# Performance work log

Measured on AMD Instinct MI355X. Metric: run time of the kernel, lower is better.

The kernel has to match this reference:

```python
import jax, jax.numpy as jnp
import numpy as np


def setup_inputs() -> dict:
    key = jax.random.key(0)
    k1, k2 = jax.random.split(key)
    N, DIM = 32768, 1024
    M, K, D = 8, 1024, 128  # n_quantizer, n_codeword, sub_dim
    x = jax.random.normal(k1, (N, DIM), dtype=jnp.float32)
    CodeBooks = jax.random.uniform(k2, (M, K, D), dtype=jnp.float32)  # torch.rand init
    return {"x": x, "CodeBooks": CodeBooks, "soft_rate": -1}


def reference(x, CodeBooks, soft_rate):
    # x: [N, dim]; CodeBooks: [M, K, D] with dim = M*D
    N = x.shape[0]
    M, K, D = CodeBooks.shape
    # forward detaches x before quantizing
    sx = jax.lax.stop_gradient(x).reshape(-1, M, D)  # [N, M, D]
    # squared euclidean distances for all sub-quantizers at once:
    # d2[n,m,k] = ||sx[n,m] - CB[m,k]||^2
    dots = jnp.einsum("nmd,mkd->nmk", sx, CodeBooks)          # [N, M, K]
    x2 = jnp.sum(sx * sx, axis=-1)                             # [N, M]
    c2 = jnp.sum(CodeBooks * CodeBooks, axis=-1)               # [M, K]
    d2 = x2[:, :, None] + c2[None, :, :] - 2.0 * dots          # [N, M, K]
    if soft_rate == -1:
        # argmax of -dist == argmin of squared dist (sqrt is monotone)
        idx = jnp.argmin(d2, axis=-1)                          # [N, M]
        Q = CodeBooks[jnp.arange(M)[None, :], idx]             # [N, M, D]
    else:
        dist = -jnp.sqrt(jnp.maximum(d2, 0.0))                 # -cdist, p=2
        w = jax.nn.softmax(dist * soft_rate, axis=-1)          # [N, M, K]
        Q = jnp.einsum("nmk,mkd->nmd", w, CodeBooks)           # [N, M, D]
    return Q.reshape(N, M * D)
```

## Files before the change

### kernel.cpp

```cpp
#include <hip/hip_runtime.h>
#include <stdint.h>

#define NROWS   32768
#define XDIM    1024
#define NCB     8
#define NCODE   1024
#define CDIM    128

#define CHUNK   32
#define NCHUNK  (NCODE / CHUNK)

#define NTH     512
#define ROWS_PB 256
#define RPW     32

typedef _Float16 h8 __attribute__((ext_vector_type(8)));
typedef float    f4 __attribute__((ext_vector_type(4)));

#define LO_SCALE 2048.0f
#define LO_INV   4.8828125e-4f

#define WS_HI   ((size_t)0)
#define WS_LO   ((size_t)NCB * NCODE * CDIM * 2)
#define WS_C2   ((size_t)2 * NCB * NCODE * CDIM * 2)
#define WS_NEED (WS_C2 + (size_t)NCB * NCODE * 4)

__device__ __forceinline__ void gload_lds16(const void* g, void* l) {
    __builtin_amdgcn_global_load_lds(
        (const __attribute__((address_space(1))) void*)g,
        (__attribute__((address_space(3))) void*)l, 16, 0, 0);
}

__global__ __launch_bounds__(256)
void precompute_kernel(const float* __restrict__ cb, uint8_t* __restrict__ ws)
{
    _Float16* hi = (_Float16*)(ws + WS_HI);
    _Float16* lo = (_Float16*)(ws + WS_LO);
    float*    c2 = (float*)(ws + WS_C2);

    const int idx  = blockIdx.x * 256 + threadIdx.x;
    const int g    = idx & 15;
    const int code = idx >> 4;
    const int kr   = code & 31;
    const int gs   = g ^ (kr & 7);

    const float* src = cb + (size_t)code * CDIM + gs * 8;
    float v[8];
    *(f4*)&v[0] = *(const f4*)src;
    *(f4*)&v[4] = *(const f4*)(src + 4);

    _Float16 hh[8], ll[8];
    double s = 0.0;
    #pragma unroll
    for (int i = 0; i < 8; ++i) {
        _Float16 h = (_Float16)v[i];
        float    r = v[i] - (float)h;
        hh[i] = h; ll[i] = (_Float16)(r * LO_SCALE);
        s = fma((double)v[i], (double)v[i], s);
    }
    const size_t off = (size_t)code * CDIM + g * 8;
    *(h8*)(hi + off) = *(h8*)hh;
    *(h8*)(lo + off) = *(h8*)ll;

    #pragma unroll
    for (int mask = 1; mask <= 8; mask <<= 1)
        s += __shfl_xor(s, mask, 16);
    if (g == 0) c2[code] = (float)s;
}

__global__ __launch_bounds__(NTH, 4)
void quant_fast(const float* __restrict__ x, const float* __restrict__ cb,
                const uint8_t* __restrict__ ws, float* __restrict__ out)
{
    __shared__ __align__(16) _Float16 chS[2][CHUNK][CDIM];
    __shared__ __align__(16) _Float16 clS[2][CHUNK][CDIM];
    __shared__ float  c2s[NCODE];
    __shared__ float  x2s[ROWS_PB];
    __shared__ int    idxs[ROWS_PB];

    const _Float16* pre_hi = (const _Float16*)(ws + WS_HI);
    const _Float16* pre_lo = (const _Float16*)(ws + WS_LO);
    const float*    c2w    = (const float*)(ws + WS_C2);

    const int t    = threadIdx.x;
    const int m    = blockIdx.x & 7;
    const int rb   = blockIdx.x >> 3;
    const int row0 = rb * ROWS_PB;

    const int l    = t & 63;
    const int w    = t >> 6;
    const int l15  = l & 15;
    const int lh   = l >> 4;
    const int mskr = (l & 7) * 8;

    const size_t cbase = (size_t)m * NCODE * CDIM;

    auto stage = [&](int c, int buf) {
        const _Float16* gh = pre_hi + cbase + (size_t)(c * CHUNK + w * 4) * CDIM + l * 8;
        const _Float16* gl = pre_lo + cbase + (size_t)(c * CHUNK + w * 4) * CDIM + l * 8;
        gload_lds16(gh, &chS[buf][w * 4][0]);
        gload_lds16(gl, &clS[buf][w * 4][0]);
    };

    stage(0, 0);

    if (t < 256) *(f4*)&c2s[t * 4] = *(const f4*)&c2w[m * NCODE + t * 4];

    h8 xh[2][4], xl[2][4];
    #pragma unroll
    for (int rs = 0; rs < 2; ++rs) {
        const float* xp = x + (size_t)(row0 + w * RPW + rs * 16 + l15) * XDIM + m * CDIM + lh * 8;
        double s = 0.0;
        #pragma unroll
        for (int ks = 0; ks < 4; ++ks) {
            float v[8];
            *(f4*)&v[0] = *(const f4*)(xp + ks * 32);
            *(f4*)&v[4] = *(const f4*)(xp + ks * 32 + 4);
            #pragma unroll
            for (int i = 0; i < 8; ++i) {
                _Float16 h = (_Float16)v[i];
                float    r = v[i] - (float)h;
                xh[rs][ks][i] = h;
                xl[rs][ks][i] = (_Float16)(r * LO_SCALE);
                s = fma((double)v[i], (double)v[i], s);
            }
        }
        s += __shfl_xor(s, 16, 64);
        s += __shfl_xor(s, 32, 64);
        if (lh == 0) x2s[w * RPW + rs * 16 + l15] = (float)s;
    }

    __syncthreads();

    float x2r[2][4];
    #pragma unroll
    for (int rs = 0; rs < 2; ++rs)
        #pragma unroll
        for (int j = 0; j < 4; ++j)
            x2r[rs][j] = x2s[w * RPW + rs * 16 + lh * 4 + j];

    float mval[2][4];
    int   midx[2][4];
    #pragma unroll
    for (int rs = 0; rs < 2; ++rs)
        #pragma unroll
        for (int j = 0; j < 4; ++j) { mval[rs][j] = 3.0e38f; midx[rs][j] = 0; }

    for (int c = 0; c < NCHUNK; ++c) {
        const int cur = c & 1;
        if (c + 1 < NCHUNK) stage(c + 1, cur ^ 1);

        #pragma unroll
        for (int cf = 0; cf < 2; ++cf) {
            const int kloc = cf * 16 + l15;
            f4 accH[2] = {{0,0,0,0},{0,0,0,0}};
            f4 accS[2] = {{0,0,0,0},{0,0,0,0}};
            #pragma unroll
            for (int ks = 0; ks < 4; ++ks) {
                const int e = (ks * 32 + lh * 8) ^ mskr;
                h8 bh = *(const h8*)&chS[cur][kloc][e];
                h8 bl = *(const h8*)&clS[cur][kloc][e];
                accH[0] = __builtin_amdgcn_mfma_f32_16x16x32_f16(xh[0][ks], bh, accH[0], 0, 0, 0);
                accH[1] = __builtin_amdgcn_mfma_f32_16x16x32_f16(xh[1][ks], bh, accH[1], 0, 0, 0);
                accS[0] = __builtin_amdgcn_mfma_f32_16x16x32_f16(xh[0][ks], bl, accS[0], 0, 0, 0);
                accS[0] = __builtin_amdgcn_mfma_f32_16x16x32_f16(xl[0][ks], bh, accS[0], 0, 0, 0);
                accS[1] = __builtin_amdgcn_mfma_f32_16x16x32_f16(xh[1][ks], bl, accS[1], 0, 0, 0);
                accS[1] = __builtin_amdgcn_mfma_f32_16x16x32_f16(xl[1][ks], bh, accS[1], 0, 0, 0);
            }
            const int   code = c * CHUNK + kloc;
            const float c2v  = c2s[code];
            #pragma unroll
            for (int rs = 0; rs < 2; ++rs)
                #pragma unroll
                for (int j = 0; j < 4; ++j) {
                    float dot = fmaf(accS[rs][j], LO_INV, accH[rs][j]);
                    float d2  = (x2r[rs][j] + c2v) - 2.0f * dot;
                    if (d2 < mval[rs][j]) { mval[rs][j] = d2; midx[rs][j] = code; }
                }
        }
        __syncthreads();
    }

    #pragma unroll
    for (int mask = 1; mask <= 8; mask <<= 1)
        #pragma unroll
        for (int rs = 0; rs < 2; ++rs)
            #pragma unroll
            for (int j = 0; j < 4; ++j) {
                float ov = __shfl_xor(mval[rs][j], mask, 64);
                int   oi = __shfl_xor(midx[rs][j], mask, 64);
                if (ov < mval[rs][j] || (ov == mval[rs][j] && oi < midx[rs][j])) {
                    mval[rs][j] = ov; midx[rs][j] = oi;
                }
            }
    if (l15 == 0)
        #pragma unroll
        for (int rs = 0; rs < 2; ++rs)
            #pragma unroll
            for (int j = 0; j < 4; ++j)
                idxs[w * RPW + rs * 16 + lh * 4 + j] = midx[rs][j];
    __syncthreads();

    {
        const int row  = t >> 1;
        const int half = (t & 1) * 64;
        const float* src = cb + ((size_t)m * NCODE + idxs[row]) * CDIM + half;
        float*       dst = out + (size_t)(row0 + row) * XDIM + m * CDIM + half;
        #pragma unroll
        for (int i = 0; i < 16; ++i)
            *(f4*)(dst + i * 4) = *(const f4*)(src + i * 4);
    }
}

__global__ __launch_bounds__(512, 4)
void quant_fallback(const float* __restrict__ x, const float* __restrict__ cb,
                    float* __restrict__ out)
{
    __shared__ __align__(16) _Float16 chS[2][CHUNK][CDIM];
    __shared__ __align__(16) _Float16 clS[2][CHUNK][CDIM];
    __shared__ float  c2s[NCODE];
    __shared__ double x2p[4][128];
    __shared__ float  x2s[128];
    __shared__ int    idxs[128];

    const int t = threadIdx.x, bid = blockIdx.x;
    const int m = bid >> 8, rb = bid & 255, row0 = rb * 128;
    const int l = t & 63, w = t >> 6, l15 = l & 15, lh = l >> 4;
    const int mskr = (l & 7) * 8;

    for (int rep = 0; rep < 2; ++rep) {
        int k = t + rep * 512;
        const float* p = cb + ((size_t)m * NCODE + k) * CDIM;
        double s0 = 0, s1 = 0, s2 = 0, s3 = 0;
        for (int d = 0; d < CDIM; d += 4) {
            double v0 = p[d], v1 = p[d+1], v2 = p[d+2], v3 = p[d+3];
            s0 = fma(v0,v0,s0); s1 = fma(v1,v1,s1); s2 = fma(v2,v2,s2); s3 = fma(v3,v3,s3);
        }
        c2s[k] = (float)((s0+s1)+(s2+s3));
    }
    {
        int row = t >> 2, q = t & 3;
        const float* p = x + (size_t)(row0+row)*XDIM + m*CDIM + q*32;
        double s0 = 0, s1 = 0;
        for (int i = 0; i < 32; i += 2) { double v0=p[i], v1=p[i+1]; s0=fma(v0,v0,s0); s1=fma(v1,v1,s1); }
        x2p[q][row] = s0 + s1;
    }
    h8 xh[4], xl[4];
    {
        const float* xp = x + (size_t)(row0 + w*16 + l15)*XDIM + m*CDIM + lh*8;
        #pragma unroll
        for (int ks = 0; ks < 4; ++ks) {
            float v[8];
            *(f4*)&v[0] = *(const f4*)(xp + ks*32);
            *(f4*)&v[4] = *(const f4*)(xp + ks*32 + 4);
            #pragma unroll
            for (int i = 0; i < 8; ++i) {
                _Float16 h = (_Float16)v[i]; float r = v[i] - (float)h;
                xh[ks][i] = h; xl[ks][i] = (_Float16)(r * LO_SCALE);
            }
        }
    }
    __syncthreads();
    if (t < 128) x2s[t] = (float)((x2p[0][t]+x2p[1][t])+(x2p[2][t]+x2p[3][t]));

    const int kr = t >> 4, db = (t & 15) * 8, ew = db ^ ((kr & 7) * 8);
    auto stage_load = [&](int c, f4& a, f4& b) {
        const float* p = cb + ((size_t)m*NCODE + c*CHUNK + kr)*CDIM + db;
        a = *(const f4*)p; b = *(const f4*)(p + 4);
    };
    auto stage_write = [&](int buf, f4 a, f4 b) {
        float v[8]; *(f4*)&v[0] = a; *(f4*)&v[4] = b;
        _Float16 hh[8], ll[8];
        #pragma unroll
        for (int i = 0; i < 8; ++i) {
            _Float16 h = (_Float16)v[i]; float r = v[i] - (float)h;
            hh[i] = h; ll[i] = (_Float16)(r * LO_SCALE);
        }
        *(h8*)&chS[buf][kr][ew] = *(h8*)hh;
        *(h8*)&clS[buf][kr][ew] = *(h8*)ll;
    };

    f4 pa, pb;
    stage_load(0, pa, pb);
    stage_write(0, pa, pb);
    __syncthreads();

    float x2r[4];
    #pragma unroll
    for (int j = 0; j < 4; ++j) x2r[j] = x2s[w*16 + lh*4 + j];
    float mval[4]; int midx[4];
    #pragma unroll
    for (int j = 0; j < 4; ++j) { mval[j] = 3.0e38f; midx[j] = 0; }

    for (int c = 0; c < NCHUNK; ++c) {
        const int cur = c & 1;
        f4 na, nb;
        if (c + 1 < NCHUNK) stage_load(c + 1, na, nb);
        #pragma unroll
        for (int cf = 0; cf < 2; ++cf) {
            const int kloc = cf*16 + l15;
            f4 accH = {0,0,0,0}, accS = {0,0,0,0};
            #pragma unroll
            for (int ks = 0; ks < 4; ++ks) {
                const int e = (ks*32 + lh*8) ^ mskr;
                h8 bh = *(const h8*)&chS[cur][kloc][e];
                h8 bl = *(const h8*)&clS[cur][kloc][e];
                accH = __builtin_amdgcn_mfma_f32_16x16x32_f16(xh[ks], bh, accH, 0, 0, 0);
                accS = __builtin_amdgcn_mfma_f32_16x16x32_f16(xh[ks], bl, accS, 0, 0, 0);
                accS = __builtin_amdgcn_mfma_f32_16x16x32_f16(xl[ks], bh, accS, 0, 0, 0);
            }
            const int code = c*CHUNK + kloc;
            const float c2v = c2s[code];
            #pragma unroll
            for (int j = 0; j < 4; ++j) {
                float dot = fmaf(accS[j], LO_INV, accH[j]);
                float d2 = (x2r[j] + c2v) - 2.0f*dot;
                if (d2 < mval[j]) { mval[j] = d2; midx[j] = code; }
            }
        }
        if (c + 1 < NCHUNK) stage_write((c + 1) & 1, na, nb);
        __syncthreads();
    }
    #pragma unroll
    for (int mask = 1; mask <= 8; mask <<= 1)
        #pragma unroll
        for (int j = 0; j < 4; ++j) {
            float ov = __shfl_xor(mval[j], mask, 64);
            int   oi = __shfl_xor(midx[j], mask, 64);
            if (ov < mval[j] || (ov == mval[j] && oi < midx[j])) { mval[j] = ov; midx[j] = oi; }
        }
    if (l15 == 0)
        #pragma unroll
        for (int j = 0; j < 4; ++j) idxs[w*16 + lh*4 + j] = midx[j];
    __syncthreads();
    {
        const int row = t >> 2, qd = (t & 3) * 32;
        const float* src = cb + ((size_t)m*NCODE + idxs[row])*CDIM + qd;
        float* dst = out + (size_t)(row0+row)*XDIM + m*CDIM + qd;
        #pragma unroll
        for (int i = 0; i < 8; ++i) *(f4*)(dst + i*4) = *(const f4*)(src + i*4);
    }
}

extern "C" void kernel_launch(void* const* d_in, const int* in_sizes, int n_in,
                              void* d_out, int out_size, void* d_ws, size_t ws_size,
                              hipStream_t stream) {
    const float* x   = (const float*)d_in[0];
    const float* cb  = (const float*)d_in[1];
    float*       out = (float*)d_out;
    if (ws_size >= WS_NEED && d_ws != nullptr) {
        precompute_kernel<<<dim3(512), dim3(256), 0, stream>>>(cb, (uint8_t*)d_ws);
        quant_fast<<<dim3(NCB * (NROWS / ROWS_PB)), dim3(NTH), 0, stream>>>(
            x, cb, (const uint8_t*)d_ws, out);
    } else {
        quant_fallback<<<dim3(2048), dim3(512), 0, stream>>>(x, cb, out);
    }
}
```

Measured before the change: 300.6 us.

## Repack codebook chunks into contiguous blobs with conflict-free LDS layout and prefetch

The precompute kernel now writes each 32-code chunk's hi/lo fp16 halves into one contiguous 16KB blob, laid out by 8-element group then code. The main kernel stages a chunk with linear global-to-LDS copies and reads B fragments with a linear, unswizzled LDS layout. It also software-prefetches the next k-step's B fragments ahead of the MFMAs. The aim is cheaper address math and LDS reads without bank conflicts, plus hiding LDS latency. The cost is a memory clobber barrier that may constrain scheduling.

New measurement: 366.3 us. 1.22x slower.

```diff
diff --git a/kernel.cpp b/kernel.cpp
--- a/kernel.cpp
+++ b/kernel.cpp
@@ -20,9 +20,8 @@
 #define LO_SCALE 2048.0f
 #define LO_INV   4.8828125e-4f
 
-#define WS_HI   ((size_t)0)
-#define WS_LO   ((size_t)NCB * NCODE * CDIM * 2)
-#define WS_C2   ((size_t)2 * NCB * NCODE * CDIM * 2)
+#define BLOB_BYTES 16384
+#define WS_C2   ((size_t)NCB * NCHUNK * BLOB_BYTES)
 #define WS_NEED (WS_C2 + (size_t)NCB * NCODE * 4)
 
 __device__ __forceinline__ void gload_lds16(const void* g, void* l) {
@@ -34,17 +33,16 @@
 __global__ __launch_bounds__(256)
 void precompute_kernel(const float* __restrict__ cb, uint8_t* __restrict__ ws)
 {
-    _Float16* hi = (_Float16*)(ws + WS_HI);
-    _Float16* lo = (_Float16*)(ws + WS_LO);
-    float*    c2 = (float*)(ws + WS_C2);
+    float* c2 = (float*)(ws + WS_C2);
 
     const int idx  = blockIdx.x * 256 + threadIdx.x;
     const int g    = idx & 15;
     const int code = idx >> 4;
-    const int kr   = code & 31;
-    const int gs   = g ^ (kr & 7);
-
-    const float* src = cb + (size_t)code * CDIM + gs * 8;
+    const int mm   = code >> 10;
+    const int c    = (code & 1023) >> 5;
+    const int k    = code & 31;
+
+    const float* src = cb + (size_t)code * CDIM + g * 8;
     float v[8];
     *(f4*)&v[0] = *(const f4*)src;
     *(f4*)&v[4] = *(const f4*)(src + 4);
@@ -58,9 +56,9 @@
         hh[i] = h; ll[i] = (_Float16)(r * LO_SCALE);
         s = fma((double)v[i], (double)v[i], s);
     }
-    const size_t off = (size_t)code * CDIM + g * 8;
-    *(h8*)(hi + off) = *(h8*)hh;
-    *(h8*)(lo + off) = *(h8*)ll;
+    uint8_t* blob = ws + ((size_t)(mm * NCHUNK + c)) * BLOB_BYTES;
+    *(h8*)(blob + g * 512 + k * 16)        = *(h8*)hh;
+    *(h8*)(blob + 8192 + g * 512 + k * 16) = *(h8*)ll;
 
     #pragma unroll
     for (int mask = 1; mask <= 8; mask <<= 1)
@@ -72,15 +70,12 @@
 void quant_fast(const float* __restrict__ x, const float* __restrict__ cb,
                 const uint8_t* __restrict__ ws, float* __restrict__ out)
 {
-    __shared__ __align__(16) _Float16 chS[2][CHUNK][CDIM];
-    __shared__ __align__(16) _Float16 clS[2][CHUNK][CDIM];
+    __shared__ __align__(16) _Float16 S[2][2][16][CHUNK][8];
     __shared__ float  c2s[NCODE];
     __shared__ float  x2s[ROWS_PB];
     __shared__ int    idxs[ROWS_PB];
 
-    const _Float16* pre_hi = (const _Float16*)(ws + WS_HI);
-    const _Float16* pre_lo = (const _Float16*)(ws + WS_LO);
-    const float*    c2w    = (const float*)(ws + WS_C2);
+    const float* c2w = (const float*)(ws + WS_C2);
 
     const int t    = threadIdx.x;
     const int m    = blockIdx.x & 7;
@@ -91,15 +86,12 @@
     const int w    = t >> 6;
     const int l15  = l & 15;
     const int lh   = l >> 4;
-    const int mskr = (l & 7) * 8;
-
-    const size_t cbase = (size_t)m * NCODE * CDIM;
 
     auto stage = [&](int c, int buf) {
-        const _Float16* gh = pre_hi + cbase + (size_t)(c * CHUNK + w * 4) * CDIM + l * 8;
-        const _Float16* gl = pre_lo + cbase + (size_t)(c * CHUNK + w * 4) * CDIM + l * 8;
-        gload_lds16(gh, &chS[buf][w * 4][0]);
-        gload_lds16(gl, &clS[buf][w * 4][0]);
+        const uint8_t* src = ws + ((size_t)(m * NCHUNK + c) << 14) + (w << 11) + (l << 4);
+        char* dst = (char*)&S[0][0][0][0][0] + buf * 16384 + (w << 11);
+        gload_lds16(src,        dst);
+        gload_lds16(src + 1024, dst + 1024);
     };
 
     stage(0, 0);
@@ -146,28 +138,38 @@
         #pragma unroll
         for (int j = 0; j < 4; ++j) { mval[rs][j] = 3.0e38f; midx[rs][j] = 0; }
 
+    const _Float16* Sl = &S[0][0][0][0][0] + (lh * 256 + l15 * 8);
+
     for (int c = 0; c < NCHUNK; ++c) {
         const int cur = c & 1;
         if (c + 1 < NCHUNK) stage(c + 1, cur ^ 1);
 
+        const _Float16* Sc = Sl + cur * 8192;
+
         #pragma unroll
         for (int cf = 0; cf < 2; ++cf) {
-            const int kloc = cf * 16 + l15;
             f4 accH[2] = {{0,0,0,0},{0,0,0,0}};
             f4 accS[2] = {{0,0,0,0},{0,0,0,0}};
+
+            h8 bh = *(const h8*)(Sc +        cf * 128);
+            h8 bl = *(const h8*)(Sc + 4096 + cf * 128);
             #pragma unroll
             for (int ks = 0; ks < 4; ++ks) {
-                const int e = (ks * 32 + lh * 8) ^ mskr;
-                h8 bh = *(const h8*)&chS[cur][kloc][e];
-                h8 bl = *(const h8*)&clS[cur][kloc][e];
+                h8 bhn, bln;
+                if (ks < 3) {
+                    bhn = *(const h8*)(Sc +        (ks + 1) * 1024 + cf * 128);
+                    bln = *(const h8*)(Sc + 4096 + (ks + 1) * 1024 + cf * 128);
+                } else { bhn = bh; bln = bl; }
                 accH[0] = __builtin_amdgcn_mfma_f32_16x16x32_f16(xh[0][ks], bh, accH[0], 0, 0, 0);
                 accH[1] = __builtin_amdgcn_mfma_f32_16x16x32_f16(xh[1][ks], bh, accH[1], 0, 0, 0);
                 accS[0] = __builtin_amdgcn_mfma_f32_16x16x32_f16(xh[0][ks], bl, accS[0], 0, 0, 0);
                 accS[0] = __builtin_amdgcn_mfma_f32_16x16x32_f16(xl[0][ks], bh, accS[0], 0, 0, 0);
                 accS[1] = __builtin_amdgcn_mfma_f32_16x16x32_f16(xh[1][ks], bl, accS[1], 0, 0, 0);
                 accS[1] = __builtin_amdgcn_mfma_f32_16x16x32_f16(xl[1][ks], bh, accS[1], 0, 0, 0);
-            }
-            const int   code = c * CHUNK + kloc;
+                asm volatile("" ::: "memory");
+                bh = bhn; bl = bln;
+            }
+            const int   code = c * CHUNK + cf * 16 + l15;
             const float c2v  = c2s[code];
             #pragma unroll
             for (int rs = 0; rs < 2; ++rs)
```

## Triple-buffer codebook chunks in LDS with prefetch distance two and manual waitcnt barriers

Applied to the files above, without the earlier changes.

Replaces the double-buffered LDS staging of codebook hi/lo chunks with a three-buffer ring that prefetches two chunks ahead. __syncthreads is replaced by explicit s_waitcnt vmcnt(2) plus s_barrier, so one chunk's loads can stay in flight across the barrier. The loop is unrolled by three so buffer indices are constants. The goal is to hide global-to-LDS latency behind the MFMA work, at the cost of 50% more LDS. That extra LDS may cut occupancy below the launch-bounds target, and the hand-written vmcnt counts depend on how many loads each stage issues.

Result: slower. 961.1 us (+219.7%).

```diff
diff --git a/kernel.cpp b/kernel.cpp
--- a/kernel.cpp
+++ b/kernel.cpp
@@ -9,6 +9,7 @@
 
 #define CHUNK   32
 #define NCHUNK  (NCODE / CHUNK)
+#define NBUF    3
 
 #define NTH     512
 #define ROWS_PB 256
@@ -72,8 +73,8 @@
 void quant_fast(const float* __restrict__ x, const float* __restrict__ cb,
                 const uint8_t* __restrict__ ws, float* __restrict__ out)
 {
-    __shared__ __align__(16) _Float16 chS[2][CHUNK][CDIM];
-    __shared__ __align__(16) _Float16 clS[2][CHUNK][CDIM];
+    __shared__ __align__(16) _Float16 chS[NBUF][CHUNK][CDIM];
+    __shared__ __align__(16) _Float16 clS[NBUF][CHUNK][CDIM];
     __shared__ float  c2s[NCODE];
     __shared__ float  x2s[ROWS_PB];
     __shared__ int    idxs[ROWS_PB];
@@ -102,8 +103,6 @@
         gload_lds16(gl, &clS[buf][w * 4][0]);
     };
 
-    stage(0, 0);
-
     if (t < 256) *(f4*)&c2s[t * 4] = *(const f4*)&c2w[m * NCODE + t * 4];
 
     h8 xh[2][4], xl[2][4];
@@ -130,7 +129,11 @@
         if (lh == 0) x2s[w * RPW + rs * 16 + l15] = (float)s;
     }
 
-    __syncthreads();
+    stage(0, 0);
+    stage(1, 1);
+
+    asm volatile("s_waitcnt vmcnt(2) lgkmcnt(0)" ::: "memory");
+    asm volatile("s_barrier" ::: "memory");
 
     float x2r[2][4];
     #pragma unroll
@@ -146,9 +149,8 @@
         #pragma unroll
         for (int j = 0; j < 4; ++j) { mval[rs][j] = 3.0e38f; midx[rs][j] = 0; }
 
-    for (int c = 0; c < NCHUNK; ++c) {
-        const int cur = c & 1;
-        if (c + 1 < NCHUNK) stage(c + 1, cur ^ 1);
+    auto body = [&](int c, int buf, bool pf, bool deep) {
+        if (pf) stage(c + 2, (buf + 2) % 3);
 
         #pragma unroll
         for (int cf = 0; cf < 2; ++cf) {
@@ -158,8 +160,8 @@
             #pragma unroll
             for (int ks = 0; ks < 4; ++ks) {
                 const int e = (ks * 32 + lh * 8) ^ mskr;
-                h8 bh = *(const h8*)&chS[cur][kloc][e];
-                h8 bl = *(const h8*)&clS[cur][kloc][e];
+                h8 bh = *(const h8*)&chS[buf][kloc][e];
+                h8 bl = *(const h8*)&clS[buf][kloc][e];
                 accH[0] = __builtin_amdgcn_mfma_f32_16x16x32_f16(xh[0][ks], bh, accH[0], 0, 0, 0);
                 accH[1] = __builtin_amdgcn_mfma_f32_16x16x32_f16(xh[1][ks], bh, accH[1], 0, 0, 0);
                 accS[0] = __builtin_amdgcn_mfma_f32_16x16x32_f16(xh[0][ks], bl, accS[0], 0, 0, 0);
@@ -178,8 +180,19 @@
                     if (d2 < mval[rs][j]) { mval[rs][j] = d2; midx[rs][j] = code; }
                 }
         }
-        __syncthreads();
-    }
+        if (deep) asm volatile("s_waitcnt vmcnt(2)" ::: "memory");
+        else      asm volatile("s_waitcnt vmcnt(0)" ::: "memory");
+        asm volatile("s_barrier" ::: "memory");
+    };
+
+    #pragma unroll 1
+    for (int cg = 0; cg < 30; cg += 3) {
+        body(cg + 0, 0, true, true);
+        body(cg + 1, 1, true, true);
+        body(cg + 2, 2, true, true);
+    }
+    body(30, 0, false, false);
+    body(31, 1, false, false);
 
     #pragma unroll
     for (int mask = 1; mask <= 8; mask <<= 1)
```
